# Kernel optimization log

Hardware: AMD Instinct MI355X
Metric: run time of the kernel (lower is better)

## Reference

```python
import jax, jax.numpy as jnp
import numpy as np

OUT = 7            # output_size per dim
RATIO = 2          # sampling_ratio
CANON_S = 160.0    # canonical_scale
CANON_L = 4.0      # canonical_level
EPS = 1e-6
K_MIN, K_MAX = 2, 5                      # from scales 1/4 .. 1/32
SCALES = (0.25, 0.125, 0.0625, 0.03125)  # inferred vs 256^3 image


def _coords(start, bsz):
    # start,bsz: [N] -> sample coords [N, OUT*RATIO]
    offs = (jnp.arange(OUT)[:, None] + (jnp.arange(RATIO) + 0.5) / RATIO).reshape(-1)
    return start[:, None] + offs[None, :] * bsz[:, None]


def _axis(c, dim):
    # torchvision border handling: zero outside [-1, dim], clamp inside
    valid = ((c > -1.0) & (c < dim)).astype(c.dtype)
    cc = jnp.clip(c, 0.0, dim - 1.0)
    lo = jnp.floor(cc).astype(jnp.int32)
    hi = jnp.minimum(lo + 1, int(dim) - 1)
    frac = cc - lo
    return lo, hi, (1.0 - frac) * valid, frac * valid


def roi_align_3d(feat, batch_idx, boxes, scale):
    # feat [B,C,X,Y,Z]; boxes [N,6] = (x1,y1,z1,x2,y2,z2) in image coords
    N = boxes.shape[0]
    C = feat.shape[1]
    dims = feat.shape[2:]
    start = boxes[:, :3] * scale
    size = jnp.maximum(boxes[:, 3:] * scale - start, 1.0)
    bsz = size / OUT  # [N,3] bin sizes
    f = jnp.transpose(feat, (0, 2, 3, 4, 1))  # [B,X,Y,Z,C]
    ax = [_axis(_coords(start[:, d], bsz[:, d]), float(dims[d])) for d in range(3)]
    b = batch_idx
    acc = jnp.zeros((N, OUT * RATIO, OUT * RATIO, OUT * RATIO, C), feat.dtype)
    for ix, wx in ((ax[0][0], ax[0][2]), (ax[0][1], ax[0][3])):
        for iy, wy in ((ax[1][0], ax[1][2]), (ax[1][1], ax[1][3])):
            for iz, wz in ((ax[2][0], ax[2][2]), (ax[2][1], ax[2][3])):
                v = f[b[:, None, None, None], ix[:, :, None, None],
                      iy[:, None, :, None], iz[:, None, None, :]]  # [N,Sx,Sy,Sz,C]
                w = wx[:, :, None, None] * wy[:, None, :, None] * wz[:, None, None, :]
                acc = acc + w[..., None] * v
    # average sampling points within each bin
    acc = acc.reshape(N, OUT, RATIO, OUT, RATIO, OUT, RATIO, C).mean(axis=(2, 4, 6))
    return jnp.transpose(acc, (0, 4, 1, 2, 3))  # [N,C,OUT,OUT,OUT]


def level_map(boxes):
    vol = ((boxes[:, 3] - boxes[:, 0]) * (boxes[:, 4] - boxes[:, 1])
           * (boxes[:, 5] - boxes[:, 2]))
    s = jnp.cbrt(vol)
    lvl = jnp.floor(CANON_L + jnp.log2(s / CANON_S) + EPS)
    return jnp.clip(lvl, K_MIN, K_MAX).astype(jnp.int32) - K_MIN


def setup_inputs() -> dict:
    key = jax.random.key(0)
    ks = jax.random.split(key, 6)
    N, C = 256, 64
    feat0 = jax.random.normal(ks[0], (1, C, 64, 64, 64), jnp.float32)
    feat1 = jax.random.normal(ks[1], (1, C, 32, 32, 32), jnp.float32)
    feat2 = jax.random.normal(ks[2], (1, C, 16, 16, 16), jnp.float32)
    feat3 = jax.random.normal(ks[3], (1, C, 8, 8, 8), jnp.float32)
    sz = 10.0 + jax.random.uniform(ks[4], (N, 3)) * 240.0   # edge lengths
    p1 = jax.random.uniform(ks[5], (N, 3)) * (256.0 - sz)
    boxes = jnp.concatenate([p1, p1 + sz], axis=1)  # valid (x1<x2 etc.) in 256^3 image
    return {"feat0": feat0, "feat1": feat1, "feat2": feat2, "feat3": feat3, "boxes": boxes}


def reference(feat0, feat1, feat2, feat3, boxes):
    feats = (feat0, feat1, feat2, feat3)
    levels = level_map(boxes)
    b = jnp.zeros(boxes.shape[0], dtype=jnp.int32)  # single image -> all batch id 0
    out = jnp.zeros((boxes.shape[0], feat0.shape[1], OUT, OUT, OUT), feat0.dtype)
    for l, (feat, sc) in enumerate(zip(feats, SCALES)):
        pooled = roi_align_3d(feat, b, boxes, sc)
        mask = (levels == l).astype(pooled.dtype)[:, None, None, None, None]
        out = out + mask * pooled
    return out
```

## Files before the change

kernel.cpp:

```cpp
#include <hip/hip_runtime.h>
#include <math.h>

#define OUT 7
#define NVOX 343
#define NCHUNK 22

typedef unsigned short u16;
typedef unsigned int u32;

__device__ __forceinline__ u16 f32_to_bf16(float f) {
    u32 u = __float_as_uint(f);
    u32 r = (u + 0x7fffu + ((u >> 16) & 1u)) >> 16;
    return (u16)r;
}
__device__ __forceinline__ float bf16_to_f32(u16 h) {
    return __uint_as_float(((u32)h) << 16);
}

__device__ __forceinline__ void axis_samp(float c, float fdim, int dim,
                                          int& lo, float& w0, float& w1) {
    float valid = (c > -1.0f && c < fdim) ? 1.0f : 0.0f;
    float cc = fminf(fmaxf(c, 0.0f), fdim - 1.0f);
    lo = (int)floorf(cc);
    float fr = cc - (float)lo;
    w0 = (1.0f - fr) * valid;
    w1 = fr * valid;
}

__device__ __forceinline__ void box_setup(const float* bp,
                                          int d0, int d1, int d2_, int d3,
                                          int& l, int& dim, float& fdim,
                                          float& st0, float& st1, float& st2,
                                          float& bs0, float& bs1, float& bs2) {
    float b0 = bp[0], b1 = bp[1], b2 = bp[2];
    float b3 = bp[3], b4 = bp[4], b5 = bp[5];
    float vol = (b3 - b0) * (b4 - b1) * (b5 - b2);
    float s = cbrtf(vol);
    float lvl = floorf(4.0f + log2f(s / 160.0f) + 1e-6f);
    lvl = fminf(fmaxf(lvl, 2.0f), 5.0f);
    l = (int)lvl - 2;
    float scale;
    if (l == 0)      { dim = d0;  scale = 0.25f;    }
    else if (l == 1) { dim = d1;  scale = 0.125f;   }
    else if (l == 2) { dim = d2_; scale = 0.0625f;  }
    else             { dim = d3;  scale = 0.03125f; }
    fdim = (float)dim;
    st0 = b0 * scale; st1 = b1 * scale; st2 = b2 * scale;
    float e0 = fmaxf(b3 * scale - st0, 1.0f);
    float e1 = fmaxf(b4 * scale - st1, 1.0f);
    float e2 = fmaxf(b5 * scale - st2, 1.0f);
    bs0 = e0 * (1.0f / OUT); bs1 = e1 * (1.0f / OUT); bs2 = e2 * (1.0f / OUT);
}

#define LDSF 11776
#define FBLK 512

__global__ __launch_bounds__(FBLK) void roi_align_fallback_kernel(
    const float* __restrict__ f0, const float* __restrict__ f1,
    const float* __restrict__ f2, const float* __restrict__ f3,
    const float* __restrict__ boxes, float* __restrict__ out,
    int N, int C, int d0, int d1, int d2_, int d3)
{
    __shared__ float lds[LDSF];
    const int c   = blockIdx.x;
    const int n   = blockIdx.y;
    const int tid = threadIdx.x;

    int l, dim; float fdim, st0, st1, st2, bs0, bs1, bs2;
    box_setup(boxes + n * 6, d0, d1, d2_, d3,
              l, dim, fdim, st0, st1, st2, bs0, bs1, bs2);
    const float* f = (l == 0) ? f0 : (l == 1) ? f1 : (l == 2) ? f2 : f3;

    const int dsq = dim * dim;
    const size_t dcube = (size_t)dim * dsq;
    const float* fc = f + (size_t)c * dcube;

    int x0 = (int)floorf(fminf(fmaxf(st0 + 0.25f * bs0, 0.0f), fdim - 1.0f));
    int x1 = min((int)floorf(fminf(fmaxf(st0 + 6.75f * bs0, 0.0f), fdim - 1.0f)) + 1, dim - 1);
    int y0 = (int)floorf(fminf(fmaxf(st1 + 0.25f * bs1, 0.0f), fdim - 1.0f));
    int y1 = min((int)floorf(fminf(fmaxf(st1 + 6.75f * bs1, 0.0f), fdim - 1.0f)) + 1, dim - 1);
    int z0 = (int)floorf(fminf(fmaxf(st2 + 0.25f * bs2, 0.0f), fdim - 1.0f));
    int z1 = min((int)floorf(fminf(fmaxf(st2 + 6.75f * bs2, 0.0f), fdim - 1.0f)) + 1, dim - 1);

    int nx = x1 - x0 + 1, ny = y1 - y0 + 1, nz = z1 - z0 + 1;
    int nzp = nz + 1;
    int nynzp = ny * nzp;
    int nrows = nx * ny;
    int nregp = nrows * nzp;

    int xl[2], yl[2], zl[2];
    float xw0[2], xw1[2], yw0[2], yw1[2], zw0[2], zw1[2];
    if (tid < NVOX) {
        int oz = tid % OUT;
        int oy = (tid / OUT) % OUT;
        int ox = tid / (OUT * OUT);
        #pragma unroll
        for (int r = 0; r < 2; ++r) {
            float off = 0.25f + 0.5f * (float)r;
            axis_samp(st0 + ((float)ox + off) * bs0, fdim, dim, xl[r], xw0[r], xw1[r]);
            axis_samp(st1 + ((float)oy + off) * bs1, fdim, dim, yl[r], yw0[r], yw1[r]);
            axis_samp(st2 + ((float)oz + off) * bs2, fdim, dim, zl[r], zw0[r], zw1[r]);
        }
    }

    if (nregp <= LDSF) {
        float rnzp = 1.0f / (float)nzp;
        float rny  = 1.0f / (float)ny;
        for (int e = tid; e < nregp; e += FBLK) {
            int row = (int)((float)e * rnzp);
            int zz = e - row * nzp;
            if (zz < 0)        { row -= 1; zz += nzp; }
            else if (zz >= nzp){ row += 1; zz -= nzp; }
            int rx = (int)((float)row * rny);
            int ry = row - rx * ny;
            if (ry < 0)        { rx -= 1; ry += ny; }
            else if (ry >= ny) { rx += 1; ry -= ny; }
            int zsrc = min(zz, nz - 1);
            lds[e] = fc[((size_t)(x0 + rx) * dim + (y0 + ry)) * dim + (z0 + zsrc)];
        }
        __syncthreads();

        if (tid < NVOX) {
            int XL[2], XH[2], YL[2], YH[2], ZL[2];
            #pragma unroll
            for (int r = 0; r < 2; ++r) {
                XL[r] = (xl[r] - x0) * nynzp;
                XH[r] = (min(xl[r] + 1, dim - 1) - x0) * nynzp;
                YL[r] = (yl[r] - y0) * nzp;
                YH[r] = (min(yl[r] + 1, dim - 1) - y0) * nzp;
                ZL[r] = zl[r] - z0;
            }
            float acc = 0.0f;
            #pragma unroll
            for (int rx2 = 0; rx2 < 2; ++rx2) {
                #pragma unroll
                for (int ry2 = 0; ry2 < 2; ++ry2) {
                    #pragma unroll
                    for (int rz2 = 0; rz2 < 2; ++rz2) {
                        const float* pll = lds + (XL[rx2] + YL[ry2] + ZL[rz2]);
                        const float* plh = lds + (XL[rx2] + YH[ry2] + ZL[rz2]);
                        const float* phl = lds + (XH[rx2] + YL[ry2] + ZL[rz2]);
                        const float* phh = lds + (XH[rx2] + YH[ry2] + ZL[rz2]);
                        float wz0 = zw0[rz2], wz1 = zw1[rz2];
                        float vx0 = yw0[ry2] * (wz0 * pll[0] + wz1 * pll[1])
                                  + yw1[ry2] * (wz0 * plh[0] + wz1 * plh[1]);
                        float vx1 = yw0[ry2] * (wz0 * phl[0] + wz1 * phl[1])
                                  + yw1[ry2] * (wz0 * phh[0] + wz1 * phh[1]);
                        acc += xw0[rx2] * vx0 + xw1[rx2] * vx1;
                    }
                }
            }
            out[((size_t)n * C + c) * NVOX + tid] = acc * 0.125f;
        }
    } else {
        if (tid < NVOX) {
            float acc = 0.0f;
            #pragma unroll
            for (int rx2 = 0; rx2 < 2; ++rx2) {
                const float* pxl = fc + (size_t)xl[rx2] * dsq;
                const float* pxh = fc + (size_t)min(xl[rx2] + 1, dim - 1) * dsq;
                float wx0 = xw0[rx2], wx1 = xw1[rx2];
                #pragma unroll
                for (int ry2 = 0; ry2 < 2; ++ry2) {
                    int ryl = yl[ry2] * dim;
                    int ryh = min(yl[ry2] + 1, dim - 1) * dim;
                    float wy0 = yw0[ry2], wy1 = yw1[ry2];
                    #pragma unroll
                    for (int rz2 = 0; rz2 < 2; ++rz2) {
                        int bZL = zl[rz2], bZH = min(zl[rz2] + 1, dim - 1);
                        float wz0 = zw0[rz2], wz1 = zw1[rz2];
                        float vx0 = wy0 * (wz0 * pxl[ryl + bZL] + wz1 * pxl[ryl + bZH])
                                  + wy1 * (wz0 * pxl[ryh + bZL] + wz1 * pxl[ryh + bZH]);
                        float vx1 = wy0 * (wz0 * pxh[ryl + bZL] + wz1 * pxh[ryl + bZH])
                                  + wy1 * (wz0 * pxh[ryh + bZL] + wz1 * pxh[ryh + bZH]);
                        acc += wx0 * vx0 + wx1 * vx1;
                    }
                }
            }
            out[((size_t)n * C + c) * NVOX + tid] = acc * 0.125f;
        }
    }
}

__global__ __launch_bounds__(256) void transpose_bf16_kernel(
    const float* __restrict__ f0, const float* __restrict__ f1,
    const float* __restrict__ f2, const float* __restrict__ f3,
    u16* __restrict__ ws,
    int t1, int t2, int t3,
    long S0, long S1, long S2, long S3,
    long off0, long off1, long off2, long off3)
{
    __shared__ u16 tile[64 * 65];
    int b = blockIdx.x;
    const float* src; u16* dst; long S; int tloc;
    if (b < t1)      { src = f0; dst = ws + off0; S = S0; tloc = b; }
    else if (b < t2) { src = f1; dst = ws + off1; S = S1; tloc = b - t1; }
    else if (b < t3) { src = f2; dst = ws + off2; S = S2; tloc = b - t2; }
    else             { src = f3; dst = ws + off3; S = S3; tloc = b - t3; }

    long s0 = (long)tloc * 64;
    int lane  = threadIdx.x & 63;
    int chunk = threadIdx.x >> 6;
    #pragma unroll
    for (int k = 0; k < 16; ++k) {
        int ch = chunk * 16 + k;
        tile[lane * 65 + ch] = f32_to_bf16(src[(size_t)ch * S + s0 + lane]);
    }
    __syncthreads();
    #pragma unroll
    for (int k = 0; k < 16; ++k) {
        int s = chunk * 16 + k;
        dst[(s0 + s) * 64 + lane] = tile[s * 65 + lane];
    }
}

__global__ __launch_bounds__(256, 4) void roi_align_cl_kernel(
    const u16* __restrict__ ws, const float* __restrict__ boxes,
    float* __restrict__ out, int N, int C,
    int d0, int d1, int d2_, int d3,
    long off0, long off1, long off2, long off3)
{
    __shared__ float4 axtab[16 * 6];
    __shared__ float ldsout[64 * 17];

    const int n    = blockIdx.x;
    const int cb   = blockIdx.y * 16;
    const int tid  = threadIdx.x;
    const int quad = tid & 15;
    const int slot = tid >> 4;

    int l, dim; float fdim, st0, st1, st2, bs0, bs1, bs2;
    box_setup(boxes + n * 6, d0, d1, d2_, d3,
              l, dim, fdim, st0, st1, st2, bs0, bs1, bs2);
    const u16* ftl = ws + ((l == 0) ? off0 : (l == 1) ? off1 : (l == 2) ? off2 : off3)
                   + quad * 4;
    const int dsq = dim * dim;

    if (quad == 0) {
        int v = min(cb + slot, NVOX - 1);
        int o2 = v % OUT;
        int t7 = v / OUT;
        int o1 = t7 % OUT;
        int o0 = t7 / OUT;
        const int stA[3] = { dsq * 64, dim * 64, 64 };
        const float oA[3] = { (float)o0, (float)o1, (float)o2 };
        const float sA[3] = { st0, st1, st2 };
        const float bA[3] = { bs0, bs1, bs2 };
        #pragma unroll
        for (int a = 0; a < 3; ++a) {
            #pragma unroll
            for (int r = 0; r < 2; ++r) {
                float cc = sA[a] + (oA[a] + (0.25f + 0.5f * (float)r)) * bA[a];
                int lo; float w0, w1;
                axis_samp(cc, fdim, dim, lo, w0, w1);
                float4 e;
                e.x = __int_as_float(lo * stA[a]);
                e.y = __int_as_float(min(lo + 1, dim - 1) * stA[a]);
                e.z = w0; e.w = w1;
                axtab[slot * 6 + a * 2 + r] = e;
            }
        }
    }
    __syncthreads();

    const bool active = (cb + slot) < NVOX;
    if (active) {
        const float4* tb = &axtab[slot * 6];
        float4 ex0 = tb[0], ex1 = tb[1], ey0 = tb[2], ey1 = tb[3], ez0 = tb[4], ez1 = tb[5];
        float xw[4] = { ex0.z, ex0.w, ex1.z, ex1.w };
        int   xo[4] = { __float_as_int(ex0.x), __float_as_int(ex0.y),
                        __float_as_int(ex1.x), __float_as_int(ex1.y) };
        float yw[4] = { ey0.z, ey0.w, ey1.z, ey1.w };
        int   yo[4] = { __float_as_int(ey0.x), __float_as_int(ey0.y),
                        __float_as_int(ey1.x), __float_as_int(ey1.y) };
        float zw[4] = { ez0.z, ez0.w, ez1.z, ez1.w };
        int   zq[4] = { __float_as_int(ez0.x), __float_as_int(ez0.y),
                        __float_as_int(ez1.x), __float_as_int(ez1.y) };

        float4 acc = { 0.f, 0.f, 0.f, 0.f };
        #pragma unroll
        for (int i2 = 0; i2 < 4; ++i2) {
            float wxv = xw[i2];
            int a1 = xo[i2];
            #pragma unroll
            for (int j2 = 0; j2 < 4; ++j2) {
                float wxy = wxv * yw[j2];
                int a2 = a1 + yo[j2];
                #pragma unroll
                for (int k2 = 0; k2 < 4; ++k2) {
                    float w = wxy * zw[k2];
                    const ushort4 v = *(const ushort4*)(ftl + a2 + zq[k2]);
                    acc.x += w * bf16_to_f32(v.x);
                    acc.y += w * bf16_to_f32(v.y);
                    acc.z += w * bf16_to_f32(v.z);
                    acc.w += w * bf16_to_f32(v.w);
                }
            }
        }
        int chb = quad * 4;
        ldsout[(chb + 0) * 17 + slot] = acc.x * 0.125f;
        ldsout[(chb + 1) * 17 + slot] = acc.y * 0.125f;
        ldsout[(chb + 2) * 17 + slot] = acc.z * 0.125f;
        ldsout[(chb + 3) * 17 + slot] = acc.w * 0.125f;
    }
    __syncthreads();

    int nv = min(16, NVOX - cb);
    #pragma unroll
    for (int k = 0; k < 4; ++k) {
        int flat = k * 256 + tid;
        int ch = flat >> 4, vs = flat & 15;
        if (vs < nv)
            out[((size_t)n * C + ch) * NVOX + cb + vs] = ldsout[ch * 17 + vs];
    }
}

extern "C" void kernel_launch(void* const* d_in, const int* in_sizes, int n_in,
                              void* d_out, int out_size, void* d_ws, size_t ws_size,
                              hipStream_t stream) {
    const float* f0 = (const float*)d_in[0];
    const float* f1 = (const float*)d_in[1];
    const float* f2 = (const float*)d_in[2];
    const float* f3 = (const float*)d_in[3];
    const float* boxes = (const float*)d_in[4];
    float* out = (float*)d_out;

    int N = in_sizes[4] / 6;
    int C = out_size / (N * NVOX);

    auto cdim = [&](int sz) {
        int per_c = sz / C;
        return (int)(cbrtf((float)per_c) + 0.5f);
    };
    int d0 = cdim(in_sizes[0]);
    int d1 = cdim(in_sizes[1]);
    int d2 = cdim(in_sizes[2]);
    int d3 = cdim(in_sizes[3]);

    long S0 = (long)d0 * d0 * d0, S1 = (long)d1 * d1 * d1;
    long S2 = (long)d2 * d2 * d2, S3 = (long)d3 * d3 * d3;
    long off0 = 0, off1 = S0 * C, off2 = off1 + S1 * C, off3 = off2 + S2 * C;
    size_t need = (size_t)(off3 + S3 * C) * sizeof(u16);

    bool fast = (C == 64) && (ws_size >= need) &&
                (S0 % 64 == 0) && (S1 % 64 == 0) && (S2 % 64 == 0) && (S3 % 64 == 0);

    if (fast) {
        u16* ws = (u16*)d_ws;
        int t1 = (int)(S0 / 64);
        int t2 = t1 + (int)(S1 / 64);
        int t3 = t2 + (int)(S2 / 64);
        int tt = t3 + (int)(S3 / 64);
        transpose_bf16_kernel<<<tt, 256, 0, stream>>>(f0, f1, f2, f3, ws,
                                                      t1, t2, t3,
                                                      S0, S1, S2, S3,
                                                      off0, off1, off2, off3);
        dim3 grid(N, NCHUNK);
        roi_align_cl_kernel<<<grid, 256, 0, stream>>>(ws, boxes, out, N, C,
                                                      d0, d1, d2, d3,
                                                      off0, off1, off2, off3);
    } else {
        dim3 grid(C, N);
        roi_align_fallback_kernel<<<grid, FBLK, 0, stream>>>(f0, f1, f2, f3, boxes, out,
                                                             N, C, d0, d1, d2, d3);
    }
}
```

Baseline: 159.4 us.

## Merge duplicate axis samples and skip zero-weight taps via compacted tap list

Per output voxel, the two sample points per axis are merged when they hit the same feature index, and zero-weight taps are dropped, producing a compacted list of (offset, weight) taps built cooperatively in LDS. The gather loop then walks this variable-length list with software-pipelined grouped loads instead of the fixed 64-tap unrolled loop. This cuts redundant global loads for small boxes and out-of-range samples, at the cost of an extra LDS pass, a second barrier and a variable-trip loop.

New measurement: 145.9 us. -8.5%, faster.

```diff
diff --git a/kernel.cpp b/kernel.cpp
--- a/kernel.cpp
+++ b/kernel.cpp
@@ -214,13 +214,54 @@
     }
 }
 
+
+#define LSTRIDE 66
+
+struct Grp { float w0, w1, w2, w3; ushort4 v0, v1, v2, v3; };
+
+__device__ __forceinline__ Grp issue_grp(const int2* L, int g,
+                                         const char* base, int qoff) {
+    int4 a = *(const int4*)(L + (g << 2));
+    int4 b = *(const int4*)(L + (g << 2) + 2);
+    Grp r;
+    r.w0 = __int_as_float(a.y); r.v0 = *(const ushort4*)(base + (a.x + qoff));
+    r.w1 = __int_as_float(a.w); r.v1 = *(const ushort4*)(base + (a.z + qoff));
+    r.w2 = __int_as_float(b.y); r.v2 = *(const ushort4*)(base + (b.x + qoff));
+    r.w3 = __int_as_float(b.w); r.v3 = *(const ushort4*)(base + (b.z + qoff));
+    return r;
+}
+
+__device__ __forceinline__ void consume_grp(const Grp& g, float4& acc) {
+    acc.x = fmaf(g.w0, bf16_to_f32(g.v0.x), acc.x);
+    acc.y = fmaf(g.w0, bf16_to_f32(g.v0.y), acc.y);
+    acc.z = fmaf(g.w0, bf16_to_f32(g.v0.z), acc.z);
+    acc.w = fmaf(g.w0, bf16_to_f32(g.v0.w), acc.w);
+    acc.x = fmaf(g.w1, bf16_to_f32(g.v1.x), acc.x);
+    acc.y = fmaf(g.w1, bf16_to_f32(g.v1.y), acc.y);
+    acc.z = fmaf(g.w1, bf16_to_f32(g.v1.z), acc.z);
+    acc.w = fmaf(g.w1, bf16_to_f32(g.v1.w), acc.w);
+    acc.x = fmaf(g.w2, bf16_to_f32(g.v2.x), acc.x);
+    acc.y = fmaf(g.w2, bf16_to_f32(g.v2.y), acc.y);
+    acc.z = fmaf(g.w2, bf16_to_f32(g.v2.z), acc.z);
+    acc.w = fmaf(g.w2, bf16_to_f32(g.v2.w), acc.w);
+    acc.x = fmaf(g.w3, bf16_to_f32(g.v3.x), acc.x);
+    acc.y = fmaf(g.w3, bf16_to_f32(g.v3.y), acc.y);
+    acc.z = fmaf(g.w3, bf16_to_f32(g.v3.z), acc.z);
+    acc.w = fmaf(g.w3, bf16_to_f32(g.v3.w), acc.w);
+}
+
 __global__ __launch_bounds__(256, 4) void roi_align_cl_kernel(
     const u16* __restrict__ ws, const float* __restrict__ boxes,
     float* __restrict__ out, int N, int C,
     int d0, int d1, int d2_, int d3,
     long off0, long off1, long off2, long off3)
 {
-    __shared__ float4 axtab[16 * 6];
+    __shared__ int2  lst[16 * LSTRIDE];
+    __shared__ float axw[16][3][4];
+    __shared__ int   axo[16][3][4];
+    __shared__ int   hdrN[16];
+    __shared__ int   hdrM[16];
+    __shared__ float hdrR[16][2];
     __shared__ float ldsout[64 * 17];
 
     const int n    = blockIdx.x;
@@ -232,69 +273,102 @@
     int l, dim; float fdim, st0, st1, st2, bs0, bs1, bs2;
     box_setup(boxes + n * 6, d0, d1, d2_, d3,
               l, dim, fdim, st0, st1, st2, bs0, bs1, bs2);
-    const u16* ftl = ws + ((l == 0) ? off0 : (l == 1) ? off1 : (l == 2) ? off2 : off3)
-                   + quad * 4;
+    const long loff = (l == 0) ? off0 : (l == 1) ? off1 : (l == 2) ? off2 : off3;
     const int dsq = dim * dim;
 
-    if (quad == 0) {
-        int v = min(cb + slot, NVOX - 1);
+    if (tid < 16) {
+        const int s = tid;
+        int v = min(cb + s, NVOX - 1);
         int o2 = v % OUT;
         int t7 = v / OUT;
         int o1 = t7 % OUT;
         int o0 = t7 / OUT;
-        const int stA[3] = { dsq * 64, dim * 64, 64 };
-        const float oA[3] = { (float)o0, (float)o1, (float)o2 };
-        const float sA[3] = { st0, st1, st2 };
-        const float bA[3] = { bs0, bs1, bs2 };
+        const int   strB[3] = { dsq * 128, dim * 128, 128 };
+        const float oA[3]   = { (float)o0, (float)o1, (float)o2 };
+        const float sA[3]   = { st0, st1, st2 };
+        const float bA[3]   = { bs0, bs1, bs2 };
+        int m3[3];
         #pragma unroll
         for (int a = 0; a < 3; ++a) {
-            #pragma unroll
-            for (int r = 0; r < 2; ++r) {
-                float cc = sA[a] + (oA[a] + (0.25f + 0.5f * (float)r)) * bA[a];
-                int lo; float w0, w1;
-                axis_samp(cc, fdim, dim, lo, w0, w1);
-                float4 e;
-                e.x = __int_as_float(lo * stA[a]);
-                e.y = __int_as_float(min(lo + 1, dim - 1) * stA[a]);
-                e.z = w0; e.w = w1;
-                axtab[slot * 6 + a * 2 + r] = e;
-            }
+            int lo0, lo1; float w00, w01, w10, w11;
+            axis_samp(sA[a] + (oA[a] + 0.25f) * bA[a], fdim, dim, lo0, w00, w01);
+            axis_samp(sA[a] + (oA[a] + 0.75f) * bA[a], fdim, dim, lo1, w10, w11);
+            int hi0 = min(lo0 + 1, dim - 1);
+            int hi1 = min(lo1 + 1, dim - 1);
+            int sa, sb; float qa, qb;
+            if (hi0 <= lo1) { sa = hi0; qa = w01; sb = lo1; qb = w10; }
+            else            { sa = lo1; qa = w10; sb = hi0; qb = w01; }
+            int m = 0;
+            int cur = lo0; float wacc = w00;
+            if (sa == cur) wacc += qa;
+            else {
+                if (wacc > 0.0f) { axw[s][a][m] = wacc; axo[s][a][m] = cur * strB[a]; ++m; }
+                cur = sa; wacc = qa;
+            }
+            if (sb == cur) wacc += qb;
+            else {
+                if (wacc > 0.0f) { axw[s][a][m] = wacc; axo[s][a][m] = cur * strB[a]; ++m; }
+                cur = sb; wacc = qb;
+            }
+            if (hi1 == cur) wacc += w11;
+            else {
+                if (wacc > 0.0f) { axw[s][a][m] = wacc; axo[s][a][m] = cur * strB[a]; ++m; }
+                cur = hi1; wacc = w11;
+            }
+            if (wacc > 0.0f) { axw[s][a][m] = wacc; axo[s][a][m] = cur * strB[a]; ++m; }
+            m3[a] = m;
+        }
+        int nT = m3[0] * m3[1] * m3[2];
+        hdrN[s] = (nT + 7) & ~7;
+        hdrM[s] = m3[0] | (m3[1] << 8) | (m3[2] << 16);
+        hdrR[s][0] = __builtin_amdgcn_rcpf((float)max(m3[1] * m3[2], 1));
+        hdrR[s][1] = __builtin_amdgcn_rcpf((float)max(m3[2], 1));
+    }
+    __syncthreads();
+
+    if (cb + slot < NVOX) {
+        const int pm  = hdrM[slot];
+        const int my  = (pm >> 8) & 255, mz = (pm >> 16) & 255, mx = pm & 255;
+        const int myz = my * mz;
+        const int nT  = mx * myz;
+        const int nT8 = hdrN[slot];
+        const float rYZ = hdrR[slot][0], rZ = hdrR[slot][1];
+        for (int t = quad; t < nT8; t += 16) {
+            int off = 0; float w = 0.0f;
+            if (t < nT) {
+                int i   = (int)(((float)t + 0.5f) * rYZ);
+                int rem = t - i * myz;
+                int j   = (int)(((float)rem + 0.5f) * rZ);
+                int k   = rem - j * mz;
+                w   = axw[slot][0][i] * axw[slot][1][j] * axw[slot][2][k];
+                off = axo[slot][0][i] + axo[slot][1][j] + axo[slot][2][k];
+            }
+            lst[slot * LSTRIDE + t] = make_int2(off, __float_as_int(w));
         }
     }
     __syncthreads();
 
     const bool active = (cb + slot) < NVOX;
     if (active) {
-        const float4* tb = &axtab[slot * 6];
-        float4 ex0 = tb[0], ex1 = tb[1], ey0 = tb[2], ey1 = tb[3], ez0 = tb[4], ez1 = tb[5];
-        float xw[4] = { ex0.z, ex0.w, ex1.z, ex1.w };
-        int   xo[4] = { __float_as_int(ex0.x), __float_as_int(ex0.y),
-                        __float_as_int(ex1.x), __float_as_int(ex1.y) };
-        float yw[4] = { ey0.z, ey0.w, ey1.z, ey1.w };
-        int   yo[4] = { __float_as_int(ey0.x), __float_as_int(ey0.y),
-                        __float_as_int(ey1.x), __float_as_int(ey1.y) };
-        float zw[4] = { ez0.z, ez0.w, ez1.z, ez1.w };
-        int   zq[4] = { __float_as_int(ez0.x), __float_as_int(ez0.y),
-                        __float_as_int(ez1.x), __float_as_int(ez1.y) };
-
+        const char* base = (const char*)(ws + loff);
+        const int qoff   = quad * 8;
+        const int2* L    = lst + slot * LSTRIDE;
+        const int nT8    = hdrN[slot];
         float4 acc = { 0.f, 0.f, 0.f, 0.f };
-        #pragma unroll
-        for (int i2 = 0; i2 < 4; ++i2) {
-            float wxv = xw[i2];
-            int a1 = xo[i2];
-            #pragma unroll
-            for (int j2 = 0; j2 < 4; ++j2) {
-                float wxy = wxv * yw[j2];
-                int a2 = a1 + yo[j2];
-                #pragma unroll
-                for (int k2 = 0; k2 < 4; ++k2) {
-                    float w = wxy * zw[k2];
-                    const ushort4 v = *(const ushort4*)(ftl + a2 + zq[k2]);
-                    acc.x += w * bf16_to_f32(v.x);
-                    acc.y += w * bf16_to_f32(v.y);
-                    acc.z += w * bf16_to_f32(v.z);
-                    acc.w += w * bf16_to_f32(v.w);
-                }
+        if (nT8 > 0) {
+            const int nG = nT8 >> 2;
+            Grp A = issue_grp(L, 0, base, qoff);
+            int g = 1;
+            for (; g + 1 < nG; g += 2) {
+                Grp B = issue_grp(L, g, base, qoff);
+                consume_grp(A, acc);
+                A = issue_grp(L, g + 1, base, qoff);
+                consume_grp(B, acc);
+            }
+            {
+                Grp B = issue_grp(L, g, base, qoff);
+                consume_grp(A, acc);
+                consume_grp(B, acc);
             }
         }
         int chb = quad * 4;
```
